# Kernel tuning notes

Measured on AMD Instinct MI355X. Metric: run time of the kernel, lower is better.

## Reference

```python
import jax, jax.numpy as jnp
import numpy as np

B, C1, C2, NH, HC, EC, GC, NTXT, H, W = 8, 128, 128, 4, 32, 128, 512, 32, 160, 160
GA_HEADS, GA_HD, K_NN, NUM_SELECT = 4, 32, 6, 64  # graph attn: min(nh,4) heads, head_dim=C1/4
BN_EPS = 1e-5


def setup_inputs() -> dict:
    key = jax.random.key(0)
    ks = jax.random.split(key, 16)
    rn = lambda k, shape, s=0.05: jax.random.normal(k, shape, dtype=jnp.float32) * s
    return {
        'x': jax.random.normal(ks[0], (B, C1, H, W), dtype=jnp.float32),
        'guide': jax.random.normal(ks[1], (B, NTXT, GC), dtype=jnp.float32),
        'w_gm1': rn(ks[2], (C1 // 4, C1)), 'b_gm1': jnp.zeros((C1 // 4,), jnp.float32),
        'w_gm2': rn(ks[3], (GA_HEADS, C1 // 4)), 'b_gm2': jnp.zeros((GA_HEADS,), jnp.float32),
        'w_qkv': rn(ks[4], (3 * C1, C1)),
        'w_ge1': rn(ks[5], (C1 // 2, C1)), 'b_ge1': jnp.zeros((C1 // 2,), jnp.float32),
        'w_ge2': rn(ks[6], (GA_HEADS, C1 // 2)), 'b_ge2': jnp.zeros((GA_HEADS,), jnp.float32),
        'w_gl': rn(ks[7], (EC, GC)), 'b_gl': jnp.zeros((EC,), jnp.float32),
        'attn_bias': rn(ks[8], (NH,), 0.1),
        'w_proj': rn(ks[9], (C2, C1, 3, 3)),
        'bn_gamma': jnp.ones((C2,), jnp.float32), 'bn_beta': jnp.zeros((C2,), jnp.float32),
        'bn_mean': rn(ks[10], (C2,)),
        'bn_var': jax.random.uniform(ks[11], (C2,), jnp.float32, 0.5, 1.5),
    }


def _graph_attention(x, w_gm1, b_gm1, w_gm2, b_gm2, w_qkv, w_ge1, b_ge1, w_ge2, b_ge2):
    # EfficientGraphModulatedAttention.forward (eval mode, dropout off)
    b, c, h, w = x.shape
    # spatial modulation: 1x1 conv -> relu -> 1x1 conv -> sigmoid   [B,GA_HEADS,H,W]
    h1 = jax.nn.relu(jnp.einsum('bchw,oc->bohw', x, w_gm1) + b_gm1[None, :, None, None])
    sm = jax.nn.sigmoid(jnp.einsum('bchw,oc->bohw', h1, w_gm2) + b_gm2[None, :, None, None])
    # top-k important pixels per image (num_select = min(64, int(H*W*0.005)))
    imp = jnp.abs(x).mean(axis=1).reshape(b, h * w)
    _, top_idx = jax.lax.top_k(imp, NUM_SELECT)                       # [B,S]
    x_flat = x.reshape(b, c, h * w).transpose(0, 2, 1)                # [B,HW,C]
    sel = jnp.take_along_axis(x_flat, top_idx[:, :, None], axis=1)    # [B,S,C]

    def per_sample(feats):                                            # feats: [S,C]
        s = feats.shape[0]
        # KNN graph over cosine similarity; self-edges dropped (as in torch loop)
        nf = feats / jnp.clip(jnp.linalg.norm(feats, axis=1, keepdims=True), 1e-12)
        sim = nf @ nf.T                                               # [S,S]
        _, nbr = jax.lax.top_k(sim, K_NN + 1)                         # [S,K+1]
        src = jnp.repeat(jnp.arange(s), K_NN + 1)
        dst = nbr.reshape(-1)
        valid = src != dst
        # local multi-head attention over selected nodes
        qkv = (feats @ w_qkv.T).reshape(s, 3, GA_HEADS, GA_HD).transpose(1, 2, 0, 3)
        q, k, v = qkv[0], qkv[1], qkv[2]                              # [GA_HEADS,S,GA_HD]
        scores = jnp.einsum('hse,hte->hst', q, k) * (GA_HD ** -0.5)
        # edge modulation (identical for every head in the torch code)
        gw = jax.nn.relu(feats @ w_ge1.T + b_ge1) @ w_ge2.T + b_ge2   # [S,GA_HEADS]
        ew = (gw[src] * gw[dst]).mean(axis=-1)                        # [E]
        mod = jnp.zeros((s, s), feats.dtype).at[src, dst].set(jnp.where(valid, ew, 0.0))
        attn = jax.nn.softmax(scores + 0.1 * mod[None], axis=-1)
        return attn.mean(axis=(0, 2))                                 # pixel importance [S]

    pix = jax.vmap(per_sample)(sel)                                   # [B,S]
    gmw_flat = jnp.zeros((b, h * w), x.dtype).at[jnp.arange(b)[:, None], top_idx].set(pix)
    gmw = jnp.broadcast_to(gmw_flat.reshape(b, 1, h, w), (b, GA_HEADS, h, w))
    final_mod = 0.7 * sm + 0.3 * gmw
    return x * final_mod.mean(axis=1, keepdims=True)


def _forward(x, guide, w_gm1, b_gm1, w_gm2, b_gm2, w_qkv, w_ge1, b_ge1, w_ge2, b_ge2,
             w_gl, b_gl, attn_bias, w_proj, bn_gamma, bn_beta, bn_mean, bn_var):
    bs, _, h, w = x.shape
    x_mod = _graph_attention(x, w_gm1, b_gm1, w_gm2, b_gm2, w_qkv, w_ge1, b_ge1, w_ge2, b_ge2)
    x = x + 0.1 * x_mod
    g = (guide @ w_gl.T + b_gl).reshape(bs, -1, NH, HC)               # [B,n,NH,HC]
    embed = x.reshape(bs, NH, HC, h, w)                               # self.ec is None (c1==ec)
    aw = jnp.einsum('bmchw,bnmc->bmhwn', embed, g)
    aw = aw.max(axis=-1) / np.sqrt(HC).astype(np.float32)
    aw = jax.nn.sigmoid(aw + attn_bias[None, :, None, None]) * 1.0    # scale buffer == 1
    aw_single = aw.mean(axis=1)                                       # [B,H,W]
    xp = jax.lax.conv_general_dilated(x, w_proj, (1, 1), 'SAME',
                                      dimension_numbers=('NCHW', 'OIHW', 'NCHW'))
    s = bn_gamma / jnp.sqrt(bn_var + BN_EPS)                          # eval-mode BN
    xp = xp * s[None, :, None, None] + (bn_beta - bn_mean * s)[None, :, None, None]
    xp = xp.reshape(bs, NH, HC, h, w) * aw[:, :, None]
    return xp.reshape(bs, -1, h, w), aw_single


def reference(x, guide, w_gm1, b_gm1, w_gm2, b_gm2, w_qkv, w_ge1, b_ge1, w_ge2, b_ge2,
              w_gl, b_gl, attn_bias, w_proj, bn_gamma, bn_beta, bn_mean, bn_var):
    return _forward(x, guide, w_gm1, b_gm1, w_gm2, b_gm2, w_qkv, w_ge1, b_ge1, w_ge2, b_ge2,
                    w_gl, b_gl, attn_bias, w_proj, bn_gamma, bn_beta, bn_mean, bn_var)
```

## Files before the change

kernel.cpp:

```cpp
#include <hip/hip_runtime.h>
#include <hip/hip_bf16.h>
#include <math.h>

#define B_   8
#define C1_  128
#define H_   160
#define W_   160
#define HW_  25600
#define NSEL_ 64
#define BONUS_ 4.6875e-4f

typedef __attribute__((ext_vector_type(8))) unsigned short ushort8;
typedef __attribute__((ext_vector_type(8))) short short8;
typedef __attribute__((ext_vector_type(4))) float f32x4;

#define OFF_FAC 0
#define OFF_IMP 819200
#define OFF_AW4 1638400
#define OFF_G   4915200
#define OFF_TB  5046272
#define OFF_WT  5046784
#define OFF_WPK 5636608
#define OFF_XH  5931520
#define WS_NEED_FAST 58360320ULL

__device__ __forceinline__ float sigmoidf_(float v) {
    return 1.0f / (1.0f + expf(-v));
}
__device__ __forceinline__ unsigned short f2bf(float f) {
    unsigned u = __float_as_uint(f);
    return (unsigned short)((u + 0x7fffu + ((u >> 16) & 1u)) >> 16);
}
__device__ __forceinline__ float bf2f(unsigned short h) {
    return __uint_as_float(((unsigned)h) << 16);
}

__global__ void k0_wt(const float* __restrict__ wp, const float* __restrict__ gamma,
                      const float* __restrict__ beta, const float* __restrict__ mean,
                      const float* __restrict__ var, float* __restrict__ wt,
                      float* __restrict__ tb) {
    int i = blockIdx.x * 256 + threadIdx.x;
    if (i < 128) {
        float s = gamma[i] * rsqrtf(var[i] + 1e-5f);
        tb[i] = beta[i] - mean[i] * s;
    }
    if (i < 128 * 128 * 9) {
        int o  = i & 127;
        int it = i >> 7;
        float s = gamma[o] * rsqrtf(var[o] + 1e-5f);
        wt[i] = wp[o * 1152 + it] * s;
    }
}

__global__ void k0b_pack(const float* __restrict__ wp, const float* __restrict__ gamma,
                         const float* __restrict__ var, unsigned short* __restrict__ wpk) {
    int idx = blockIdx.x * 256 + threadIdx.x;
    if (idx >= 147456) return;
    int j = idx & 7, l = (idx >> 3) & 63, f = idx >> 9;
    int kstep = f >> 3, mblk = f & 7;
    int tap = kstep >> 2, icb = kstep & 3;
    int oc = mblk * 16 + (l & 15);
    int ic = icb * 32 + ((l >> 4) << 3) + j;
    float s = gamma[oc] * rsqrtf(var[oc] + 1e-5f);
    wpk[idx] = f2bf(wp[oc * 1152 + ic * 9 + tap] * s);
}

__global__ __launch_bounds__(512) void k1a_convert(const float* __restrict__ x,
                                                   float* __restrict__ imp,
                                                   unsigned short* __restrict__ xh) {
    __shared__ float red[8][256];
    const int tid = threadIdx.x;
    const int l = tid & 63, g = tid >> 6;
    const int px0 = blockIdx.x * 256;
    const int b = blockIdx.y;
    const int pxl = l * 4;
    const float* xb = x + (size_t)b * C1_ * HW_ + px0 + pxl;
    unsigned short* xrb = xh + ((size_t)(b * HW_ + px0 + pxl)) * 128 + g * 16;

    float sab0 = 0.f, sab1 = 0.f, sab2 = 0.f, sab3 = 0.f;
    ushort8 v0, v1, v2, v3;
#pragma unroll
    for (int j = 0; j < 16; ++j) {
        float4 xv = *reinterpret_cast<const float4*>(xb + (size_t)(g * 16 + j) * HW_);
        sab0 += fabsf(xv.x); sab1 += fabsf(xv.y);
        sab2 += fabsf(xv.z); sab3 += fabsf(xv.w);
        const int jj = j & 7;
        v0[jj] = f2bf(xv.x); v1[jj] = f2bf(xv.y);
        v2[jj] = f2bf(xv.z); v3[jj] = f2bf(xv.w);
        if (jj == 7) {
            const int gr = j & ~7;
            *reinterpret_cast<ushort8*>(xrb + 0 * 128 + gr) = v0;
            *reinterpret_cast<ushort8*>(xrb + 1 * 128 + gr) = v1;
            *reinterpret_cast<ushort8*>(xrb + 2 * 128 + gr) = v2;
            *reinterpret_cast<ushort8*>(xrb + 3 * 128 + gr) = v3;
        }
    }
    red[g][pxl + 0] = sab0; red[g][pxl + 1] = sab1;
    red[g][pxl + 2] = sab2; red[g][pxl + 3] = sab3;
    __syncthreads();
    if (tid < 256) {
        float s = 0.f;
#pragma unroll
        for (int gg = 0; gg < 8; ++gg) s += red[gg][tid];
        imp[b * HW_ + px0 + tid] = s * (1.f / 128.f);
    }
}

__global__ __launch_bounds__(256) void k1_mod(const float* __restrict__ x,
                                              const float* __restrict__ w_gm1,
                                              const float* __restrict__ b_gm1,
                                              const float* __restrict__ w_gm2,
                                              const float* __restrict__ b_gm2,
                                              float* __restrict__ fac,
                                              float* __restrict__ imp) {
    __shared__ float4 w1t[128 * 8];
    __shared__ float  b1s[32];
    __shared__ float  w2s[128];
    __shared__ float  b2s[4];
    const int tid = threadIdx.x;
    for (int i = tid; i < 4096; i += 256) {
        int j = i >> 7, c = i & 127;
        ((float*)w1t)[c * 32 + j] = w_gm1[i];
    }
    if (tid < 32) b1s[tid] = b_gm1[tid];
    if (tid < 128) w2s[tid] = w_gm2[tid];
    if (tid < 4) b2s[tid] = b_gm2[tid];
    __syncthreads();

    const int hw0 = blockIdx.x * 512 + tid * 2;
    const int b = blockIdx.y;
    const float* xb = x + (size_t)b * C1_ * HW_ + hw0;

    float h[2][32];
#pragma unroll
    for (int j = 0; j < 32; ++j) { h[0][j] = 0.f; h[1][j] = 0.f; }
    float sab0 = 0.f, sab1 = 0.f;
    for (int c8 = 0; c8 < 16; ++c8) {
#pragma unroll
        for (int k = 0; k < 8; ++k) {
            int c = c8 * 8 + k;
            float2 xv = *reinterpret_cast<const float2*>(xb + (size_t)c * HW_);
            sab0 += fabsf(xv.x);
            sab1 += fabsf(xv.y);
            const float4* wr = &w1t[c * 8];
#pragma unroll
            for (int j4 = 0; j4 < 8; ++j4) {
                float4 w = wr[j4];
                h[0][j4 * 4 + 0] += xv.x * w.x; h[0][j4 * 4 + 1] += xv.x * w.y;
                h[0][j4 * 4 + 2] += xv.x * w.z; h[0][j4 * 4 + 3] += xv.x * w.w;
                h[1][j4 * 4 + 0] += xv.y * w.x; h[1][j4 * 4 + 1] += xv.y * w.y;
                h[1][j4 * 4 + 2] += xv.y * w.z; h[1][j4 * 4 + 3] += xv.y * w.w;
            }
        }
    }
#pragma unroll
    for (int p = 0; p < 2; ++p) {
        float fm = 0.f;
#pragma unroll
        for (int j = 0; j < 32; ++j) h[p][j] = fmaxf(h[p][j] + b1s[j], 0.f);
#pragma unroll
        for (int m = 0; m < 4; ++m) {
            float s = b2s[m];
#pragma unroll
            for (int j = 0; j < 32; ++j) s += w2s[m * 32 + j] * h[p][j];
            fm += sigmoidf_(s);
        }
        fac[b * HW_ + hw0 + p] = 1.f + 0.07f * (fm * 0.25f);
        imp[b * HW_ + hw0 + p] = (p == 0 ? sab0 : sab1) * (1.f / 128.f);
    }
}

__device__ __forceinline__ int blockReduceSum1024(int v, int* red, int tid) {
#pragma unroll
    for (int off = 32; off >= 1; off >>= 1) v += __shfl_down(v, off);
    if ((tid & 63) == 0) red[tid >> 6] = v;
    __syncthreads();
    if (tid < 64) {
        int s = (tid < 16) ? red[tid] : 0;
#pragma unroll
        for (int off = 8; off >= 1; off >>= 1) s += __shfl_down(s, off);
        if (tid == 0) red[16] = s;
    }
    __syncthreads();
    int r = red[16];
    __syncthreads();
    return r;
}

__global__ __launch_bounds__(1024) void k2_topk(const float* __restrict__ imp,
                                                float* __restrict__ fac) {
    __shared__ int red[17];
    __shared__ int claimed;
    const int tid = threadIdx.x;
    const int b = blockIdx.x;
    unsigned u[25];
#pragma unroll
    for (int i = 0; i < 25; ++i)
        u[i] = __float_as_uint(imp[b * HW_ + i * 1024 + tid]);

    unsigned cur = 0u;
    for (int bit = 30; bit >= 0; --bit) {
        unsigned cand = cur | (1u << bit);
        int c = 0;
#pragma unroll
        for (int i = 0; i < 25; ++i) c += (u[i] >= cand) ? 1 : 0;
        int tot = blockReduceSum1024(c, red, tid);
        if (tot >= NSEL_) cur = cand;
    }
    int cg = 0;
#pragma unroll
    for (int i = 0; i < 25; ++i) cg += (u[i] > cur) ? 1 : 0;
    int tot_gt = blockReduceSum1024(cg, red, tid);
    int need = NSEL_ - tot_gt;
    if (tid == 0) claimed = 0;
    __syncthreads();
#pragma unroll
    for (int i = 0; i < 25; ++i) {
        int idx = i * 1024 + tid;
        if (u[i] > cur) {
            fac[b * HW_ + idx] += BONUS_;
        } else if (u[i] == cur) {
            int c = atomicAdd(&claimed, 1);
            if (c < need) fac[b * HW_ + idx] += BONUS_;
        }
    }
}

__global__ __launch_bounds__(128) void k3_guide(const float* __restrict__ guide,
                                                const float* __restrict__ w_gl,
                                                const float* __restrict__ b_gl,
                                                float* __restrict__ g) {
    __shared__ float gr[512];
    const int bn = blockIdx.x;
    const int tid = threadIdx.x;
    for (int i = tid; i < 512; i += 128) gr[i] = guide[bn * 512 + i];
    __syncthreads();
    const float4* w4 = (const float4*)(w_gl + (size_t)tid * 512);
    const float4* g4 = (const float4*)gr;
    float acc = b_gl[tid];
    for (int k = 0; k < 128; ++k) {
        float4 w = w4[k]; float4 v = g4[k];
        acc += w.x * v.x + w.y * v.y + w.z * v.z + w.w * v.w;
    }
    g[bn * 128 + tid] = acc;
}

__global__ __launch_bounds__(256) void k4m2_scores(const unsigned short* __restrict__ xh,
                                                   const float* __restrict__ g,
                                                   const float* __restrict__ w_gm1,
                                                   const float* __restrict__ b_gm1,
                                                   const float* __restrict__ w_gm2,
                                                   const float* __restrict__ b_gm2,
                                                   float* __restrict__ mx4,
                                                   float* __restrict__ fac) {
    __shared__ unsigned short xs[128 * 128];
    const int tid = threadIdx.x;
    const int l = tid & 63, w = tid >> 6;
    const int px0 = blockIdx.x * 128;
    const int b = blockIdx.y;

#pragma unroll
    for (int i = 0; i < 8; ++i) {
        int idx = i * 256 + tid;
        int row = idx >> 4, gg = idx & 15;
        const char* src = (const char*)(xh + ((size_t)(b * HW_ + px0 + row)) * 128
                                        + ((gg ^ (row & 7)) * 8));
        char* dst = (char*)xs + (size_t)(i * 4096 + w * 1024);
        __builtin_amdgcn_global_load_lds((const unsigned int*)src,
                                         (unsigned int*)dst, 16, 0, 0);
    }

    const int lr = l & 15, lk = l >> 4;

    short8 afr[4][2];
#pragma unroll
    for (int m = 0; m < 4; ++m)
#pragma unroll
        for (int nb = 0; nb < 2; ++nb) {
            const float* gp = g + (size_t)b * 4096 + (nb * 16 + lr) * 128
                              + m * 32 + (lk << 3);
            float4 g0 = *reinterpret_cast<const float4*>(gp);
            float4 g1 = *reinterpret_cast<const float4*>(gp + 4);
            short8 a;
            a[0] = (short)f2bf(g0.x); a[1] = (short)f2bf(g0.y);
            a[2] = (short)f2bf(g0.z); a[3] = (short)f2bf(g0.w);
            a[4] = (short)f2bf(g1.x); a[5] = (short)f2bf(g1.y);
            a[6] = (short)f2bf(g1.z); a[7] = (short)f2bf(g1.w);
            afr[m][nb] = a;
        }

    short8 w1f[2][4];
#pragma unroll
    for (int ob = 0; ob < 2; ++ob)
#pragma unroll
        for (int kb = 0; kb < 4; ++kb) {
            const float* wp = w_gm1 + (size_t)(ob * 16 + lr) * 128 + kb * 32 + (lk << 3);
            float4 g0 = *reinterpret_cast<const float4*>(wp);
            float4 g1 = *reinterpret_cast<const float4*>(wp + 4);
            short8 a;
            a[0] = (short)f2bf(g0.x); a[1] = (short)f2bf(g0.y);
            a[2] = (short)f2bf(g0.z); a[3] = (short)f2bf(g0.w);
            a[4] = (short)f2bf(g1.x); a[5] = (short)f2bf(g1.y);
            a[6] = (short)f2bf(g1.z); a[7] = (short)f2bf(g1.w);
            w1f[ob][kb] = a;
        }

    float b1r[8], w2r[4][8];
#pragma unroll
    for (int r = 0; r < 4; ++r) {
        b1r[r] = b_gm1[lk * 4 + r];
        b1r[4 + r] = b_gm1[16 + lk * 4 + r];
    }
#pragma unroll
    for (int m = 0; m < 4; ++m)
#pragma unroll
        for (int r = 0; r < 4; ++r) {
            w2r[m][r] = w_gm2[m * 32 + lk * 4 + r];
            w2r[m][4 + r] = w_gm2[m * 32 + 16 + lk * 4 + r];
        }
    const float b20 = b_gm2[0], b21 = b_gm2[1], b22 = b_gm2[2], b23 = b_gm2[3];

    __syncthreads();

#pragma unroll
    for (int pxb = 0; pxb < 2; ++pxb) {
        const int px = (w * 2 + pxb) * 16 + lr;
        float mr[4];
        f32x4 h0{0.f, 0.f, 0.f, 0.f}, h1{0.f, 0.f, 0.f, 0.f};
#pragma unroll
        for (int m = 0; m < 4; ++m) {
            int gl = (m * 4 + lk) ^ (px & 7);
            short8 bf = *reinterpret_cast<const short8*>(xs + (size_t)px * 128 + gl * 8);
            f32x4 a0{0.f, 0.f, 0.f, 0.f}, a1{0.f, 0.f, 0.f, 0.f};
            a0 = __builtin_amdgcn_mfma_f32_16x16x32_bf16(afr[m][0], bf, a0, 0, 0, 0);
            a1 = __builtin_amdgcn_mfma_f32_16x16x32_bf16(afr[m][1], bf, a1, 0, 0, 0);
            h0 = __builtin_amdgcn_mfma_f32_16x16x32_bf16(w1f[0][m], bf, h0, 0, 0, 0);
            h1 = __builtin_amdgcn_mfma_f32_16x16x32_bf16(w1f[1][m], bf, h1, 0, 0, 0);
            float v = fmaxf(fmaxf(fmaxf(a0[0], a0[1]), fmaxf(a0[2], a0[3])),
                            fmaxf(fmaxf(a1[0], a1[1]), fmaxf(a1[2], a1[3])));
            v = fmaxf(v, __shfl_xor(v, 16));
            v = fmaxf(v, __shfl_xor(v, 32));
            mr[m] = v;
        }
        float s0 = b20, s1 = b21, s2 = b22, s3 = b23;
#pragma unroll
        for (int r = 0; r < 4; ++r) {
            float hv0 = fmaxf(h0[r] + b1r[r], 0.f);
            float hv1 = fmaxf(h1[r] + b1r[4 + r], 0.f);
            s0 += w2r[0][r] * hv0 + w2r[0][4 + r] * hv1;
            s1 += w2r[1][r] * hv0 + w2r[1][4 + r] * hv1;
            s2 += w2r[2][r] * hv0 + w2r[2][4 + r] * hv1;
            s3 += w2r[3][r] * hv0 + w2r[3][4 + r] * hv1;
        }
        s0 += __shfl_xor(s0, 16); s0 += __shfl_xor(s0, 32);
        s1 += __shfl_xor(s1, 16); s1 += __shfl_xor(s1, 32);
        s2 += __shfl_xor(s2, 16); s2 += __shfl_xor(s2, 32);
        s3 += __shfl_xor(s3, 16); s3 += __shfl_xor(s3, 32);
        float fm = sigmoidf_(s0) + sigmoidf_(s1) + sigmoidf_(s2) + sigmoidf_(s3);
        if (l < 16) {
            float4 o; o.x = mr[0]; o.y = mr[1]; o.z = mr[2]; o.w = mr[3];
            int hw = px0 + (w * 2 + pxb) * 16 + l;
            *reinterpret_cast<float4*>(mx4 + (size_t)(b * HW_ + hw) * 4) = o;
            fac[b * HW_ + hw] = 1.f + 0.0175f * fm;
        }
    }
}

__global__ __launch_bounds__(256) void k4c_aw(const float* __restrict__ mx4,
                                              const float* __restrict__ fac,
                                              const float* __restrict__ attn_bias,
                                              float* __restrict__ aw4,
                                              float* __restrict__ aw_single) {
    const int hw = blockIdx.x * 256 + threadIdx.x;
    const int b = blockIdx.y;
    float4 mv = *reinterpret_cast<const float4*>(mx4 + (size_t)(b * HW_ + hw) * 4);
    float facv = fac[b * HW_ + hw] * 0.17677669529663687f;
    float b0 = attn_bias[0], b1 = attn_bias[1], b2 = attn_bias[2], b3 = attn_bias[3];
    float a0 = sigmoidf_(mv.x * facv + b0);
    float a1 = sigmoidf_(mv.y * facv + b1);
    float a2 = sigmoidf_(mv.z * facv + b2);
    float a3 = sigmoidf_(mv.w * facv + b3);
    aw4[((size_t)(b * 4 + 0)) * HW_ + hw] = a0;
    aw4[((size_t)(b * 4 + 1)) * HW_ + hw] = a1;
    aw4[((size_t)(b * 4 + 2)) * HW_ + hw] = a2;
    aw4[((size_t)(b * 4 + 3)) * HW_ + hw] = a3;
    aw_single[b * HW_ + hw] = (a0 + a1 + a2 + a3) * 0.25f;
}

__global__ __launch_bounds__(256) void k4_aw(const float* __restrict__ x,
                                             const float* __restrict__ fac,
                                             const float* __restrict__ g,
                                             const float* __restrict__ attn_bias,
                                             float* __restrict__ aw4,
                                             float* __restrict__ aw_single) {
    __shared__ float gl[4096];
    __shared__ float biass[4];
    const int tid = threadIdx.x;
    const int b = blockIdx.y;
    for (int i = tid; i < 4096; i += 256) {
        int n = i >> 7, e = i & 127;
        gl[e * 32 + n] = g[b * 4096 + i];
    }
    if (tid < 4) biass[tid] = attn_bias[tid];
    __syncthreads();
    const int hw = blockIdx.x * 256 + tid;
    const float facv = fac[b * HW_ + hw];
    const float* xb = x + (size_t)b * C1_ * HW_ + hw;
    float asum = 0.f;
#pragma unroll
    for (int m = 0; m < 4; ++m) {
        float acc[32];
#pragma unroll
        for (int n = 0; n < 32; ++n) acc[n] = 0.f;
        for (int c = 0; c < 32; ++c) {
            float xv = xb[(m * 32 + c) * HW_] * facv;
            const float4* grow = (const float4*)&gl[(m * 32 + c) * 32];
#pragma unroll
            for (int n4 = 0; n4 < 8; ++n4) {
                float4 gv = grow[n4];
                acc[n4 * 4 + 0] += xv * gv.x; acc[n4 * 4 + 1] += xv * gv.y;
                acc[n4 * 4 + 2] += xv * gv.z; acc[n4 * 4 + 3] += xv * gv.w;
            }
        }
        float mxv = acc[0];
#pragma unroll
        for (int n = 1; n < 32; ++n) mxv = fmaxf(mxv, acc[n]);
        float awv = sigmoidf_(mxv * 0.17677669529663687f + biass[m]);
        aw4[((size_t)(b * 4 + m)) * HW_ + hw] = awv;
        asum += awv;
    }
    aw_single[b * HW_ + hw] = asum * 0.25f;
}

__global__ __launch_bounds__(512, 4) void k5_mfma(const unsigned short* __restrict__ xh,
                                                  const float* __restrict__ fac,
                                                  const unsigned short* __restrict__ wpk,
                                                  const float* __restrict__ tb,
                                                  const float* __restrict__ aw4,
                                                  float* __restrict__ out) {
    __shared__ unsigned short xs[180 * 17 * 8];
    const int tid = threadIdx.x;
    const int l = tid & 63, w = tid >> 6;
    const int bx0 = blockIdx.x * 16;
    const int by0 = blockIdx.y * 8;
    const int b   = blockIdx.z;

    for (int i = tid; i < 2880; i += 512) {
        int gg = i & 15, pc = i >> 4;
        int hc = pc % 18, hr = pc / 18;
        int gy = by0 - 1 + hr, gx = bx0 - 1 + hc;
        ushort8 v;
#pragma unroll
        for (int k = 0; k < 8; ++k) v[k] = 0;
        if (gy >= 0 && gy < H_ && gx >= 0 && gx < W_) {
            int hw = gy * W_ + gx;
            v = *reinterpret_cast<const ushort8*>(xh + ((size_t)b * HW_ + hw) * 128 + gg * 8);
            float fv = fac[b * HW_ + hw];
#pragma unroll
            for (int k = 0; k < 8; ++k) v[k] = f2bf(bf2f(v[k]) * fv);
        }
        *reinterpret_cast<ushort8*>(xs + (size_t)(pc * 17 + gg) * 8) = v;
    }
    __syncthreads();

    const int qo = w >> 1;
    const int phalf = w & 1;
    const int lr = l & 15, lk = l >> 4;

    f32x4 acc[2][4];
#pragma unroll
    for (int mf = 0; mf < 2; ++mf)
#pragma unroll
        for (int nf = 0; nf < 4; ++nf)
#pragma unroll
            for (int r = 0; r < 4; ++r) acc[mf][nf][r] = 0.f;

    const unsigned short* wlane = wpk + (size_t)(qo * 2) * 512 + (size_t)l * 8;
    const unsigned short* xbase = xs + (size_t)((phalf * 4 * 18 + lr) * 17 + lk) * 8;

    short8 A0[2], A1[2];
#pragma unroll
    for (int mf = 0; mf < 2; ++mf) {
        A0[mf] = *reinterpret_cast<const short8*>(wlane + mf * 512);
        A1[mf] = *reinterpret_cast<const short8*>(wlane + 4096 + mf * 512);
    }

#pragma unroll 1
    for (int tap = 0; tap < 9; ++tap) {
        const int dy = (tap >= 6) ? 2 : (tap >= 3 ? 1 : 0);
        const int dx = tap - dy * 3;
        const unsigned short* bbase = xbase + (size_t)(((dy * 18 + dx) * 17) * 8);
        const unsigned short* wpre = wlane + (size_t)(tap * 4 + 2) * 4096;
#pragma unroll
        for (int icb = 0; icb < 4; ++icb) {
            const int k = tap * 4 + icb;
            short8 A2[2];
            if (k + 2 < 36) {
#pragma unroll
                for (int mf = 0; mf < 2; ++mf)
                    A2[mf] = *reinterpret_cast<const short8*>(wpre + (size_t)icb * 4096 + mf * 512);
            }
            short8 bf[4];
#pragma unroll
            for (int nf = 0; nf < 4; ++nf)
                bf[nf] = *reinterpret_cast<const short8*>(
                    bbase + (size_t)((nf * 18 * 17 + icb * 4) * 8));
#pragma unroll
            for (int mf = 0; mf < 2; ++mf)
#pragma unroll
                for (int nf = 0; nf < 4; ++nf)
                    acc[mf][nf] = __builtin_amdgcn_mfma_f32_16x16x32_bf16(
                        A0[mf], bf[nf], acc[mf][nf], 0, 0, 0);
            if (k < 35) {
#pragma unroll
                for (int mf = 0; mf < 2; ++mf) {
                    A0[mf] = A1[mf];
                    if (k + 2 < 36) A1[mf] = A2[mf];
                }
            }
        }
    }

    const float* awb = aw4 + (size_t)b * 4 * HW_;
    float* outb = out + (size_t)b * 128 * HW_;
    const int head = qo;
#pragma unroll
    for (int mf = 0; mf < 2; ++mf) {
        const int oc0 = qo * 32 + mf * 16 + lk * 4;
#pragma unroll
        for (int nf = 0; nf < 4; ++nf) {
            int px = phalf * 64 + nf * 16 + lr;
            int hw = (by0 + (px >> 4)) * W_ + bx0 + (px & 15);
            float aw = awb[(size_t)head * HW_ + hw];
#pragma unroll
            for (int r = 0; r < 4; ++r) {
                int oc = oc0 + r;
                outb[(size_t)oc * HW_ + hw] = (acc[mf][nf][r] + tb[oc]) * aw;
            }
        }
    }
}

__global__ __launch_bounds__(256) void k5_conv(const float* __restrict__ x,
                                               const float* __restrict__ fac,
                                               const float* __restrict__ wt,
                                               const float* __restrict__ tb,
                                               const float* __restrict__ aw4,
                                               float* __restrict__ out) {
    __shared__ float ft[18][36];
    __shared__ float xs[16][18][36];
    __shared__ float wl[16][9][32];
    const int tx = threadIdx.x;
    const int ty = threadIdx.y;
    const int tid = ty * 32 + tx;
    const int bx0 = blockIdx.x * 32;
    const int by0 = blockIdx.y * 16;
    const int m = blockIdx.z & 3;
    const int b = blockIdx.z >> 2;

    for (int i = tid; i < 18 * 34; i += 256) {
        int r = i / 34, c = i - r * 34;
        int gy = by0 - 1 + r, gx = bx0 - 1 + c;
        bool in = (gy >= 0) && (gy < H_) && (gx < W_) && (gx >= 0);
        ft[r][c] = in ? fac[b * HW_ + gy * W_ + gx] : 0.f;
    }
    float acc0[32], acc1[32];
#pragma unroll
    for (int i = 0; i < 32; ++i) { acc0[i] = 0.f; acc1[i] = 0.f; }
    __syncthreads();

    for (int icc = 0; icc < 8; ++icc) {
        const int ic0 = icc * 16;
        for (int i = tid; i < 4608; i += 256) {
            int ic = i / 288; int rem = i - ic * 288;
            int tap = rem >> 5; int oc = rem & 31;
            wl[ic][tap][oc] = wt[((ic0 + ic) * 9 + tap) * 128 + m * 32 + oc];
        }
        for (int i = tid; i < 16 * 612; i += 256) {
            int ic = i / 612; int j = i - ic * 612;
            int r = j / 34; int c = j - r * 34;
            int gy = by0 - 1 + r, gx = bx0 - 1 + c;
            int gyc = min(max(gy, 0), H_ - 1), gxc = min(max(gx, 0), W_ - 1);
            xs[ic][r][c] = x[((size_t)(b * C1_ + ic0 + ic)) * HW_ + gyc * W_ + gxc] * ft[r][c];
        }
        __syncthreads();
        for (int ic = 0; ic < 16; ++ic) {
#pragma unroll
            for (int ky = 0; ky < 3; ++ky) {
#pragma unroll
                for (int kx = 0; kx < 3; ++kx) {
                    float xv0 = xs[ic][ty + ky][tx + kx];
                    float xv1 = xs[ic][ty + 8 + ky][tx + kx];
                    const float4* wp = (const float4*)&wl[ic][ky * 3 + kx][0];
#pragma unroll
                    for (int o4 = 0; o4 < 8; ++o4) {
                        float4 wv = wp[o4];
                        acc0[o4 * 4 + 0] += xv0 * wv.x; acc0[o4 * 4 + 1] += xv0 * wv.y;
                        acc0[o4 * 4 + 2] += xv0 * wv.z; acc0[o4 * 4 + 3] += xv0 * wv.w;
                        acc1[o4 * 4 + 0] += xv1 * wv.x; acc1[o4 * 4 + 1] += xv1 * wv.y;
                        acc1[o4 * 4 + 2] += xv1 * wv.z; acc1[o4 * 4 + 3] += xv1 * wv.w;
                    }
                }
            }
        }
        __syncthreads();
    }

    const int hw0 = (by0 + ty) * W_ + bx0 + tx;
    const int hw1 = (by0 + ty + 8) * W_ + bx0 + tx;
    const float aw0 = aw4[((size_t)(b * 4 + m)) * HW_ + hw0];
    const float aw1 = aw4[((size_t)(b * 4 + m)) * HW_ + hw1];
    float* ob = out + ((size_t)(b * C1_ + m * 32)) * HW_;
#pragma unroll
    for (int oc = 0; oc < 32; ++oc) {
        float t = tb[m * 32 + oc];
        ob[oc * HW_ + hw0] = (acc0[oc] + t) * aw0;
        ob[oc * HW_ + hw1] = (acc1[oc] + t) * aw1;
    }
}

extern "C" void kernel_launch(void* const* d_in, const int* in_sizes, int n_in,
                              void* d_out, int out_size, void* d_ws, size_t ws_size,
                              hipStream_t stream) {
    const float* x        = (const float*)d_in[0];
    const float* guide    = (const float*)d_in[1];
    const float* w_gm1    = (const float*)d_in[2];
    const float* b_gm1    = (const float*)d_in[3];
    const float* w_gm2    = (const float*)d_in[4];
    const float* b_gm2    = (const float*)d_in[5];
    const float* w_gl     = (const float*)d_in[11];
    const float* b_gl     = (const float*)d_in[12];
    const float* attn_bias= (const float*)d_in[13];
    const float* w_proj   = (const float*)d_in[14];
    const float* bn_gamma = (const float*)d_in[15];
    const float* bn_beta  = (const float*)d_in[16];
    const float* bn_mean  = (const float*)d_in[17];
    const float* bn_var   = (const float*)d_in[18];

    char* wsb = (char*)d_ws;
    float* fac = (float*)(wsb + OFF_FAC);
    float* imp = (float*)(wsb + OFF_IMP);
    float* aw4 = (float*)(wsb + OFF_AW4);
    float* g   = (float*)(wsb + OFF_G);
    float* tb  = (float*)(wsb + OFF_TB);
    float* wt  = (float*)(wsb + OFF_WT);
    unsigned short* wpk = (unsigned short*)(wsb + OFF_WPK);
    unsigned short* xh  = (unsigned short*)(wsb + OFF_XH);

    float* out0 = (float*)d_out;
    float* out1 = (float*)d_out + (size_t)B_ * C1_ * HW_;
    float* mx4  = (float*)d_out;

    const bool fast = (ws_size >= WS_NEED_FAST);

    k0_wt<<<dim3(576), dim3(256), 0, stream>>>(w_proj, bn_gamma, bn_beta, bn_mean, bn_var, wt, tb);
    if (fast) {
        k0b_pack<<<dim3(576), dim3(256), 0, stream>>>(w_proj, bn_gamma, bn_var, wpk);
        k1a_convert<<<dim3(100, 8), dim3(512), 0, stream>>>(x, imp, xh);
        k3_guide<<<dim3(256), dim3(128), 0, stream>>>(guide, w_gl, b_gl, g);
        k4m2_scores<<<dim3(200, 8), dim3(256), 0, stream>>>(xh, g, w_gm1, b_gm1,
                                                            w_gm2, b_gm2, mx4, fac);
        k2_topk<<<dim3(8), dim3(1024), 0, stream>>>(imp, fac);
        k4c_aw<<<dim3(100, 8), dim3(256), 0, stream>>>(mx4, fac, attn_bias, aw4, out1);
        k5_mfma<<<dim3(10, 20, 8), dim3(512), 0, stream>>>(xh, fac, wpk, tb, aw4, out0);
    } else {
        k1_mod<<<dim3(50, 8), dim3(256), 0, stream>>>(x, w_gm1, b_gm1, w_gm2, b_gm2,
                                                      fac, imp);
        k3_guide<<<dim3(256), dim3(128), 0, stream>>>(guide, w_gl, b_gl, g);
        k2_topk<<<dim3(8), dim3(1024), 0, stream>>>(imp, fac);
        k4_aw<<<dim3(100, 8), dim3(256), 0, stream>>>(x, fac, g, attn_bias, aw4, out1);
        k5_conv<<<dim3(5, 10, B_ * 4), dim3(32, 8), 0, stream>>>(x, fac, wt, tb, aw4, out0);
    }
}
```

Before: 203.4 us.

## Split conv taps across wave halves with larger per-wave tiles and LDS reduction

The MFMA conv kernel's 8 waves are reorganized. Each wave now computes a 64-oc by 64-px tile (4x4 fragments) instead of 32x64, and the 9 taps are split between two wave groups (taps 0-3 and 4-8). The partial sums are combined through LDS over two rounds, reusing the input tile buffer. This raises arithmetic intensity per B-fragment load and reduces weight reloads per wave. The costs are more accumulator registers, an imbalanced tap split (4 vs 5), extra barriers, the LDS reduction, and only one weight prefetch stage instead of two.

```diff
diff --git a/kernel.cpp b/kernel.cpp
--- a/kernel.cpp
+++ b/kernel.cpp
@@ -463,42 +463,47 @@
     }
     __syncthreads();
 
-    const int qo = w >> 1;
-    const int phalf = w & 1;
+    const int quad = w & 3, khalf = w >> 2;
+    const int qoc = quad >> 1, qpx = quad & 1;
     const int lr = l & 15, lk = l >> 4;
 
-    f32x4 acc[2][4];
-#pragma unroll
-    for (int mf = 0; mf < 2; ++mf)
+    f32x4 acc[4][4];
+#pragma unroll
+    for (int mf = 0; mf < 4; ++mf)
 #pragma unroll
         for (int nf = 0; nf < 4; ++nf)
 #pragma unroll
             for (int r = 0; r < 4; ++r) acc[mf][nf][r] = 0.f;
 
-    const unsigned short* wlane = wpk + (size_t)(qo * 2) * 512 + (size_t)l * 8;
-    const unsigned short* xbase = xs + (size_t)((phalf * 4 * 18 + lr) * 17 + lk) * 8;
-
-    short8 A0[2], A1[2];
-#pragma unroll
-    for (int mf = 0; mf < 2; ++mf) {
-        A0[mf] = *reinterpret_cast<const short8*>(wlane + mf * 512);
-        A1[mf] = *reinterpret_cast<const short8*>(wlane + 4096 + mf * 512);
+    const int tap_lo = khalf ? 4 : 0;
+    const int tap_hi = khalf ? 9 : 4;
+    const int kend   = tap_hi * 4;
+
+    const unsigned short* wlane = wpk + (size_t)(qoc * 4) * 512 + (size_t)l * 8;
+    const unsigned short* xbase = xs + (size_t)((qpx * 4 * 18 + lr) * 17 + lk) * 8;
+
+    short8 A0[4];
+    {
+        const unsigned short* wk = wlane + (size_t)(tap_lo * 4) * 4096;
+#pragma unroll
+        for (int mf = 0; mf < 4; ++mf)
+            A0[mf] = *reinterpret_cast<const short8*>(wk + mf * 512);
     }
 
 #pragma unroll 1
-    for (int tap = 0; tap < 9; ++tap) {
+    for (int tap = tap_lo; tap < tap_hi; ++tap) {
         const int dy = (tap >= 6) ? 2 : (tap >= 3 ? 1 : 0);
         const int dx = tap - dy * 3;
         const unsigned short* bbase = xbase + (size_t)(((dy * 18 + dx) * 17) * 8);
-        const unsigned short* wpre = wlane + (size_t)(tap * 4 + 2) * 4096;
 #pragma unroll
         for (int icb = 0; icb < 4; ++icb) {
             const int k = tap * 4 + icb;
-            short8 A2[2];
-            if (k + 2 < 36) {
-#pragma unroll
-                for (int mf = 0; mf < 2; ++mf)
-                    A2[mf] = *reinterpret_cast<const short8*>(wpre + (size_t)icb * 4096 + mf * 512);
+            short8 A1[4];
+            if (k + 1 < kend) {
+                const unsigned short* wk = wlane + (size_t)(k + 1) * 4096;
+#pragma unroll
+                for (int mf = 0; mf < 4; ++mf)
+                    A1[mf] = *reinterpret_cast<const short8*>(wk + mf * 512);
             }
             short8 bf[4];
 #pragma unroll
@@ -506,36 +511,62 @@
                 bf[nf] = *reinterpret_cast<const short8*>(
                     bbase + (size_t)((nf * 18 * 17 + icb * 4) * 8));
 #pragma unroll
-            for (int mf = 0; mf < 2; ++mf)
+            for (int mf = 0; mf < 4; ++mf)
 #pragma unroll
                 for (int nf = 0; nf < 4; ++nf)
                     acc[mf][nf] = __builtin_amdgcn_mfma_f32_16x16x32_bf16(
                         A0[mf], bf[nf], acc[mf][nf], 0, 0, 0);
-            if (k < 35) {
-#pragma unroll
-                for (int mf = 0; mf < 2; ++mf) {
-                    A0[mf] = A1[mf];
-                    if (k + 2 < 36) A1[mf] = A2[mf];
+            if (k + 1 < kend) {
+#pragma unroll
+                for (int mf = 0; mf < 4; ++mf) A0[mf] = A1[mf];
+            }
+        }
+    }
+
+    float* cbuf = (float*)xs;
+#pragma unroll 1
+    for (int rnd = 0; rnd < 2; ++rnd) {
+        __syncthreads();
+        if (khalf == 1 && qoc == rnd) {
+            float* dst = cbuf + (size_t)qpx * 4352 + (size_t)l * 68;
+#pragma unroll
+            for (int mf = 0; mf < 4; ++mf)
+#pragma unroll
+                for (int nf = 0; nf < 4; ++nf)
+                    *reinterpret_cast<f32x4*>(dst + (mf * 4 + nf) * 4) = acc[mf][nf];
+        }
+        __syncthreads();
+        if (khalf == 0 && qoc == rnd) {
+            const float* src = cbuf + (size_t)qpx * 4352 + (size_t)l * 68;
+#pragma unroll
+            for (int mf = 0; mf < 4; ++mf)
+#pragma unroll
+                for (int nf = 0; nf < 4; ++nf) {
+                    f32x4 v = *reinterpret_cast<const f32x4*>(src + (mf * 4 + nf) * 4);
+                    acc[mf][nf][0] += v[0]; acc[mf][nf][1] += v[1];
+                    acc[mf][nf][2] += v[2]; acc[mf][nf][3] += v[3];
                 }
-            }
-        }
-    }
-
-    const float* awb = aw4 + (size_t)b * 4 * HW_;
-    float* outb = out + (size_t)b * 128 * HW_;
-    const int head = qo;
-#pragma unroll
-    for (int mf = 0; mf < 2; ++mf) {
-        const int oc0 = qo * 32 + mf * 16 + lk * 4;
-#pragma unroll
-        for (int nf = 0; nf < 4; ++nf) {
-            int px = phalf * 64 + nf * 16 + lr;
-            int hw = (by0 + (px >> 4)) * W_ + bx0 + (px & 15);
-            float aw = awb[(size_t)head * HW_ + hw];
-#pragma unroll
-            for (int r = 0; r < 4; ++r) {
-                int oc = oc0 + r;
-                outb[(size_t)oc * HW_ + hw] = (acc[mf][nf][r] + tb[oc]) * aw;
+        }
+    }
+
+    if (khalf == 0) {
+        const float* awb = aw4 + (size_t)b * 4 * HW_;
+        float* outb = out + (size_t)b * 128 * HW_;
+#pragma unroll
+        for (int mf = 0; mf < 4; ++mf) {
+            const int ocb = qoc * 64 + mf * 16;
+            const int oc0 = ocb + lk * 4;
+            const int head = ocb >> 5;
+#pragma unroll
+            for (int nf = 0; nf < 4; ++nf) {
+                int px = qpx * 64 + nf * 16 + lr;
+                int hw = (by0 + (px >> 4)) * W_ + bx0 + (px & 15);
+                float aw = awb[(size_t)head * HW_ + hw];
+#pragma unroll
+                for (int r = 0; r < 4; ++r) {
+                    int oc = oc0 + r;
+                    outb[(size_t)oc * HW_ + hw] = (acc[mf][nf][r] + tb[oc]) * aw;
+                }
             }
         }
     }
```

Measured after the change: 204.4 us. No clear change (+0.5%).

## Fuse prep kernels and fold attention-weight epilogue into score kernel

Applied to the files above, without the earlier changes.

Merges the weight-transform, weight-pack and guide-projection kernels into a single launch partitioned by block index. Runs top-k before the score kernel so it writes the bonus directly, then the score kernel adds its modulation term and computes the sigmoid attention weights and averaged map inline. This removes two kernel launches and the intermediate per-pixel max buffer write and read. The cost is a larger fused kernel with more registers and a reordered dependency chain.

```diff
diff --git a/kernel.cpp b/kernel.cpp
--- a/kernel.cpp
+++ b/kernel.cpp
@@ -35,34 +35,57 @@
     return __uint_as_float(((unsigned)h) << 16);
 }
 
-__global__ void k0_wt(const float* __restrict__ wp, const float* __restrict__ gamma,
-                      const float* __restrict__ beta, const float* __restrict__ mean,
-                      const float* __restrict__ var, float* __restrict__ wt,
-                      float* __restrict__ tb) {
-    int i = blockIdx.x * 256 + threadIdx.x;
-    if (i < 128) {
-        float s = gamma[i] * rsqrtf(var[i] + 1e-5f);
-        tb[i] = beta[i] - mean[i] * s;
-    }
-    if (i < 128 * 128 * 9) {
-        int o  = i & 127;
-        int it = i >> 7;
-        float s = gamma[o] * rsqrtf(var[o] + 1e-5f);
-        wt[i] = wp[o * 1152 + it] * s;
-    }
-}
-
-__global__ void k0b_pack(const float* __restrict__ wp, const float* __restrict__ gamma,
-                         const float* __restrict__ var, unsigned short* __restrict__ wpk) {
-    int idx = blockIdx.x * 256 + threadIdx.x;
-    if (idx >= 147456) return;
-    int j = idx & 7, l = (idx >> 3) & 63, f = idx >> 9;
-    int kstep = f >> 3, mblk = f & 7;
-    int tap = kstep >> 2, icb = kstep & 3;
-    int oc = mblk * 16 + (l & 15);
-    int ic = icb * 32 + ((l >> 4) << 3) + j;
-    float s = gamma[oc] * rsqrtf(var[oc] + 1e-5f);
-    wpk[idx] = f2bf(wp[oc * 1152 + ic * 9 + tap] * s);
+__global__ __launch_bounds__(256) void k_prep(const float* __restrict__ wp,
+                                              const float* __restrict__ gamma,
+                                              const float* __restrict__ beta,
+                                              const float* __restrict__ mean,
+                                              const float* __restrict__ var,
+                                              const float* __restrict__ guide,
+                                              const float* __restrict__ w_gl,
+                                              const float* __restrict__ b_gl,
+                                              float* __restrict__ wt,
+                                              float* __restrict__ tb,
+                                              unsigned short* __restrict__ wpk,
+                                              float* __restrict__ g) {
+    const int blk = blockIdx.x;
+    const int tid = threadIdx.x;
+    if (blk < 576) {
+        int i = blk * 256 + tid;
+        if (i < 128) {
+            float s = gamma[i] * rsqrtf(var[i] + 1e-5f);
+            tb[i] = beta[i] - mean[i] * s;
+        }
+        if (i < 147456) {
+            int o = i & 127, it = i >> 7;
+            float s = gamma[o] * rsqrtf(var[o] + 1e-5f);
+            wt[i] = wp[o * 1152 + it] * s;
+        }
+    } else if (blk < 1152) {
+        int idx = (blk - 576) * 256 + tid;
+        if (idx < 147456) {
+            int j = idx & 7, l = (idx >> 3) & 63, f = idx >> 9;
+            int kstep = f >> 3, mblk = f & 7;
+            int tap = kstep >> 2, icb = kstep & 3;
+            int oc = mblk * 16 + (l & 15);
+            int ic = icb * 32 + ((l >> 4) << 3) + j;
+            float s = gamma[oc] * rsqrtf(var[oc] + 1e-5f);
+            wpk[idx] = f2bf(wp[oc * 1152 + ic * 9 + tap] * s);
+        }
+    } else {
+        __shared__ float gr[2][512];
+        const int half = tid >> 7, t = tid & 127;
+        const int bn = (blk - 1152) * 2 + half;
+        for (int i = t; i < 512; i += 128) gr[half][i] = guide[bn * 512 + i];
+        __syncthreads();
+        const float4* w4 = (const float4*)(w_gl + (size_t)t * 512);
+        const float4* g4 = (const float4*)gr[half];
+        float acc = b_gl[t];
+        for (int k = 0; k < 128; ++k) {
+            float4 w = w4[k]; float4 v = g4[k];
+            acc += w.x * v.x + w.y * v.y + w.z * v.z + w.w * v.w;
+        }
+        g[bn * 128 + t] = acc;
+    }
 }
 
 __global__ __launch_bounds__(512) void k1a_convert(const float* __restrict__ x,
@@ -188,7 +211,8 @@
 }
 
 __global__ __launch_bounds__(1024) void k2_topk(const float* __restrict__ imp,
-                                                float* __restrict__ fac) {
+                                                float* __restrict__ fac,
+                                                int mode) {
     __shared__ int red[17];
     __shared__ int claimed;
     const int tid = threadIdx.x;
@@ -217,32 +241,16 @@
 #pragma unroll
     for (int i = 0; i < 25; ++i) {
         int idx = i * 1024 + tid;
+        float v = 0.f;
         if (u[i] > cur) {
-            fac[b * HW_ + idx] += BONUS_;
+            v = BONUS_;
         } else if (u[i] == cur) {
             int c = atomicAdd(&claimed, 1);
-            if (c < need) fac[b * HW_ + idx] += BONUS_;
-        }
-    }
-}
-
-__global__ __launch_bounds__(128) void k3_guide(const float* __restrict__ guide,
-                                                const float* __restrict__ w_gl,
-                                                const float* __restrict__ b_gl,
-                                                float* __restrict__ g) {
-    __shared__ float gr[512];
-    const int bn = blockIdx.x;
-    const int tid = threadIdx.x;
-    for (int i = tid; i < 512; i += 128) gr[i] = guide[bn * 512 + i];
-    __syncthreads();
-    const float4* w4 = (const float4*)(w_gl + (size_t)tid * 512);
-    const float4* g4 = (const float4*)gr;
-    float acc = b_gl[tid];
-    for (int k = 0; k < 128; ++k) {
-        float4 w = w4[k]; float4 v = g4[k];
-        acc += w.x * v.x + w.y * v.y + w.z * v.z + w.w * v.w;
-    }
-    g[bn * 128 + tid] = acc;
+            if (c < need) v = BONUS_;
+        }
+        if (mode) fac[b * HW_ + idx] = v;
+        else if (v != 0.f) fac[b * HW_ + idx] += v;
+    }
 }
 
 __global__ __launch_bounds__(256) void k4m2_scores(const unsigned short* __restrict__ xh,
@@ -251,8 +259,10 @@
                                                    const float* __restrict__ b_gm1,
                                                    const float* __restrict__ w_gm2,
                                                    const float* __restrict__ b_gm2,
-                                                   float* __restrict__ mx4,
-                                                   float* __restrict__ fac) {
+                                                   const float* __restrict__ attn_bias,
+                                                   float* __restrict__ fac,
+                                                   float* __restrict__ aw4,
+                                                   float* __restrict__ aw_single) {
     __shared__ unsigned short xs[128 * 128];
     const int tid = threadIdx.x;
     const int l = tid & 63, w = tid >> 6;
@@ -319,6 +329,8 @@
             w2r[m][4 + r] = w_gm2[m * 32 + 16 + lk * 4 + r];
         }
     const float b20 = b_gm2[0], b21 = b_gm2[1], b22 = b_gm2[2], b23 = b_gm2[3];
+    const float ab0 = attn_bias[0], ab1 = attn_bias[1];
+    const float ab2 = attn_bias[2], ab3 = attn_bias[3];
 
     __syncthreads();
 
@@ -358,33 +370,22 @@
         s3 += __shfl_xor(s3, 16); s3 += __shfl_xor(s3, 32);
         float fm = sigmoidf_(s0) + sigmoidf_(s1) + sigmoidf_(s2) + sigmoidf_(s3);
         if (l < 16) {
-            float4 o; o.x = mr[0]; o.y = mr[1]; o.z = mr[2]; o.w = mr[3];
             int hw = px0 + (w * 2 + pxb) * 16 + l;
-            *reinterpret_cast<float4*>(mx4 + (size_t)(b * HW_ + hw) * 4) = o;
-            fac[b * HW_ + hw] = 1.f + 0.0175f * fm;
-        }
-    }
-}
-
-__global__ __launch_bounds__(256) void k4c_aw(const float* __restrict__ mx4,
-                                              const float* __restrict__ fac,
-                                              const float* __restrict__ attn_bias,
-                                              float* __restrict__ aw4,
-                                              float* __restrict__ aw_single) {
-    const int hw = blockIdx.x * 256 + threadIdx.x;
-    const int b = blockIdx.y;
-    float4 mv = *reinterpret_cast<const float4*>(mx4 + (size_t)(b * HW_ + hw) * 4);
-    float facv = fac[b * HW_ + hw] * 0.17677669529663687f;
-    float b0 = attn_bias[0], b1 = attn_bias[1], b2 = attn_bias[2], b3 = attn_bias[3];
-    float a0 = sigmoidf_(mv.x * facv + b0);
-    float a1 = sigmoidf_(mv.y * facv + b1);
-    float a2 = sigmoidf_(mv.z * facv + b2);
-    float a3 = sigmoidf_(mv.w * facv + b3);
-    aw4[((size_t)(b * 4 + 0)) * HW_ + hw] = a0;
-    aw4[((size_t)(b * 4 + 1)) * HW_ + hw] = a1;
-    aw4[((size_t)(b * 4 + 2)) * HW_ + hw] = a2;
-    aw4[((size_t)(b * 4 + 3)) * HW_ + hw] = a3;
-    aw_single[b * HW_ + hw] = (a0 + a1 + a2 + a3) * 0.25f;
+            float bonus = fac[b * HW_ + hw];
+            float fv = 1.f + 0.0175f * fm + bonus;
+            fac[b * HW_ + hw] = fv;
+            float sc = fv * 0.17677669529663687f;
+            float a0 = sigmoidf_(mr[0] * sc + ab0);
+            float a1 = sigmoidf_(mr[1] * sc + ab1);
+            float a2 = sigmoidf_(mr[2] * sc + ab2);
+            float a3 = sigmoidf_(mr[3] * sc + ab3);
+            aw4[((size_t)(b * 4 + 0)) * HW_ + hw] = a0;
+            aw4[((size_t)(b * 4 + 1)) * HW_ + hw] = a1;
+            aw4[((size_t)(b * 4 + 2)) * HW_ + hw] = a2;
+            aw4[((size_t)(b * 4 + 3)) * HW_ + hw] = a3;
+            aw_single[b * HW_ + hw] = (a0 + a1 + a2 + a3) * 0.25f;
+        }
+    }
 }
 
 __global__ __launch_bounds__(256) void k4_aw(const float* __restrict__ x,
@@ -649,25 +650,23 @@
 
     float* out0 = (float*)d_out;
     float* out1 = (float*)d_out + (size_t)B_ * C1_ * HW_;
-    float* mx4  = (float*)d_out;
 
     const bool fast = (ws_size >= WS_NEED_FAST);
 
-    k0_wt<<<dim3(576), dim3(256), 0, stream>>>(w_proj, bn_gamma, bn_beta, bn_mean, bn_var, wt, tb);
+    k_prep<<<dim3(1280), dim3(256), 0, stream>>>(w_proj, bn_gamma, bn_beta, bn_mean,
+                                                 bn_var, guide, w_gl, b_gl,
+                                                 wt, tb, wpk, g);
     if (fast) {
-        k0b_pack<<<dim3(576), dim3(256), 0, stream>>>(w_proj, bn_gamma, bn_var, wpk);
         k1a_convert<<<dim3(100, 8), dim3(512), 0, stream>>>(x, imp, xh);
-        k3_guide<<<dim3(256), dim3(128), 0, stream>>>(guide, w_gl, b_gl, g);
+        k2_topk<<<dim3(8), dim3(1024), 0, stream>>>(imp, fac, 1);
         k4m2_scores<<<dim3(200, 8), dim3(256), 0, stream>>>(xh, g, w_gm1, b_gm1,
-                                                            w_gm2, b_gm2, mx4, fac);
-        k2_topk<<<dim3(8), dim3(1024), 0, stream>>>(imp, fac);
-        k4c_aw<<<dim3(100, 8), dim3(256), 0, stream>>>(mx4, fac, attn_bias, aw4, out1);
+                                                            w_gm2, b_gm2, attn_bias,
+                                                            fac, aw4, out1);
         k5_mfma<<<dim3(10, 20, 8), dim3(512), 0, stream>>>(xh, fac, wpk, tb, aw4, out0);
     } else {
         k1_mod<<<dim3(50, 8), dim3(256), 0, stream>>>(x, w_gm1, b_gm1, w_gm2, b_gm2,
                                                       fac, imp);
-        k3_guide<<<dim3(256), dim3(128), 0, stream>>>(guide, w_gl, b_gl, g);
-        k2_topk<<<dim3(8), dim3(1024), 0, stream>>>(imp, fac);
+        k2_topk<<<dim3(8), dim3(1024), 0, stream>>>(imp, fac, 0);
         k4_aw<<<dim3(100, 8), dim3(256), 0, stream>>>(x, fac, g, attn_bias, aw4, out1);
         k5_conv<<<dim3(5, 10, B_ * 4), dim3(32, 8), 0, stream>>>(x, fac, wt, tb, aw4, out0);
     }
```

Result: faster. 196.6 us (-3.3%).
